# Kernel tuning notes

Measured on AMD Instinct MI355X. Metric: run time of the kernel, lower is better.

Reference implementation:

```python
import jax, jax.numpy as jnp
import numpy as np

IN_FEATURES = 8192
OUT_FEATURES = 8192
BATCH = 64


def setup_inputs() -> dict:
    key = jax.random.key(0)
    k_x, k_mu = jax.random.split(key)
    x = jax.random.normal(k_x, (BATCH, IN_FEATURES), dtype=jnp.float32)
    # torch init: mu = rand(in,1) * out_features; sigma = ones*10; amplitude = ones; bias = zeros
    mu = jax.random.uniform(k_mu, (IN_FEATURES, 1), dtype=jnp.float32) * OUT_FEATURES
    sigma = jnp.ones((IN_FEATURES, 1), dtype=jnp.float32) * 10.0
    amplitude = jnp.ones((IN_FEATURES, 1), dtype=jnp.float32)
    bias = jnp.zeros((OUT_FEATURES,), dtype=jnp.float32)
    return {"x": x, "mu": mu, "sigma": sigma, "amplitude": amplitude, "bias": bias}


def reference(x, mu, sigma, amplitude, bias):
    out_features = bias.shape[0]
    positions = jnp.arange(out_features, dtype=x.dtype)[None, :]  # [1, out]
    diff = positions - mu                                          # [in, out]
    weight = amplitude * jnp.exp(-(diff * diff) / (2.0 * sigma * sigma))  # [in, out]
    out = x @ weight                                               # [B, out]
    return jax.nn.relu(out + bias)
```

## Files before the change

kernel.cpp:

```cpp
#include <hip/hip_runtime.h>

#define IN_F 8192
#define OUT_F 8192
#define BATCH 64
#define PASS 2048
#define TQ 64
#define CH 64

__global__ __launch_bounds__(256) void transpose_x_kern(const float* __restrict__ x,
                                                        float* __restrict__ xT) {
    __shared__ float tile[64][65];
    const int i0 = blockIdx.x * 64;
    const int tid = threadIdx.x;
#pragma unroll
    for (int u = tid; u < 64 * 64; u += 256) {
        const int b = u >> 6;
        const int i = u & 63;
        tile[i][b] = x[b * IN_F + i0 + i];
    }
    __syncthreads();
#pragma unroll
    for (int u = tid; u < 64 * 64; u += 256) {
        const int i = u >> 6;
        const int b = u & 63;
        xT[(i0 + i) * 64 + b] = tile[i][b];
    }
}

__global__ __launch_bounds__(256) void gauss_fc_kern(
    const float* __restrict__ x, const float* __restrict__ xT,
    const float* __restrict__ mu, const float* __restrict__ sigma,
    const float* __restrict__ amp, const float* __restrict__ bias,
    float* __restrict__ out, const int use_xt) {

    __shared__ float lmu[PASS];
    __shared__ float lk[PASS];
    __shared__ float lamp[PASS];
    __shared__ int   li[PASS];
    __shared__ float xs[CH][16];
    __shared__ int   cnt;

    const int tid = threadIdx.x;
    const int c = tid & 63;
    const int g = tid >> 6;
    const int tile0 = blockIdx.x * TQ;
    const int row0 = blockIdx.y * 16;
    const float colf = (float)(tile0 + c);
    const float lo = (float)tile0;
    const float hi = (float)(tile0 + TQ - 1);

    float acc0 = 0.f, acc1 = 0.f, acc2 = 0.f, acc3 = 0.f;

    for (int base = 0; base < IN_F; base += PASS) {
        if (tid == 0) cnt = 0;
        __syncthreads();

        for (int i = base + tid; i < base + PASS; i += 256) {
            const float m = mu[i];
            const float s = sigma[i];
            const float R = 8.0f * fabsf(s) + 1.0f;
            if (m >= lo - R && m <= hi + R) {
                const int p = atomicAdd(&cnt, 1);
                lmu[p] = m;
                lk[p] = -0.5f / (s * s);
                lamp[p] = amp[i];
                li[p] = i;
            }
        }
        __syncthreads();
        const int n = cnt;

        for (int cb = 0; cb < n; cb += CH) {
            const int cn = min(CH, n - cb);
            for (int u = tid; u < (cn << 4); u += 256) {
                const int ci = u >> 4;
                const int r = u & 15;
                const int i = li[cb + ci];
                xs[ci][r] = use_xt ? xT[i * 64 + row0 + r]
                                   : x[(row0 + r) * IN_F + i];
            }
            __syncthreads();

            const int g4 = g << 2;
#pragma unroll 4
            for (int j = 0; j < cn; ++j) {
                const float m = lmu[cb + j];
                const float k = lk[cb + j];
                const float a = lamp[cb + j];
                const float d = colf - m;
                const float w = a * __expf(k * d * d);
                acc0 += w * xs[j][g4 + 0];
                acc1 += w * xs[j][g4 + 1];
                acc2 += w * xs[j][g4 + 2];
                acc3 += w * xs[j][g4 + 3];
            }
            __syncthreads();
        }
    }

    const float bb = bias[tile0 + c];
    float* o = out + (size_t)(row0 + (g << 2)) * OUT_F + tile0 + c;
    float v0 = acc0 + bb;
    float v1 = acc1 + bb;
    float v2 = acc2 + bb;
    float v3 = acc3 + bb;
    o[0 * (size_t)OUT_F] = v0 > 0.f ? v0 : 0.f;
    o[1 * (size_t)OUT_F] = v1 > 0.f ? v1 : 0.f;
    o[2 * (size_t)OUT_F] = v2 > 0.f ? v2 : 0.f;
    o[3 * (size_t)OUT_F] = v3 > 0.f ? v3 : 0.f;
}

extern "C" void kernel_launch(void* const* d_in, const int* in_sizes, int n_in,
                              void* d_out, int out_size, void* d_ws, size_t ws_size,
                              hipStream_t stream) {
    const float* x     = (const float*)d_in[0];
    const float* mu    = (const float*)d_in[1];
    const float* sigma = (const float*)d_in[2];
    const float* amp   = (const float*)d_in[3];
    const float* bias  = (const float*)d_in[4];
    float* out = (float*)d_out;

    const size_t xt_bytes = (size_t)IN_F * BATCH * sizeof(float);
    const int use_xt = (ws_size >= xt_bytes) ? 1 : 0;
    float* xT = (float*)d_ws;

    if (use_xt) {
        transpose_x_kern<<<IN_F / 64, 256, 0, stream>>>(x, xT);
    }
    dim3 grid(OUT_F / TQ, 4);
    gauss_fc_kern<<<grid, 256, 0, stream>>>(x, xT, mu, sigma, amp, bias, out, use_xt);
}
```

Baseline: 97.49 us.

## Halve output tile width to double block count and vectorize mu/sigma scan

Shrinks each block's output column tile from 64 to 32, so twice as many blocks run and each thread keeps 2 batch-row accumulators instead of 4. Loads mu and sigma as float4 in the candidate-filter scan and adds a launch-bounds occupancy hint. The goal is more parallelism across CUs and a cheaper filter scan. The cost is that each Gaussian's exp is now computed per 2 rows instead of 4, so exp work per output grows, and the mu/sigma scan is repeated by twice as many blocks.

```diff
diff --git a/kernel.cpp b/kernel.cpp
--- a/kernel.cpp
+++ b/kernel.cpp
@@ -4,7 +4,8 @@
 #define OUT_F 8192
 #define BATCH 64
 #define PASS 2048
-#define TQ 64
+#define TQ 32
+#define ROWS 16
 #define CH 64
 
 __global__ __launch_bounds__(256) void transpose_x_kern(const float* __restrict__ x,
@@ -27,9 +28,9 @@
     }
 }
 
-__global__ __launch_bounds__(256) void gauss_fc_kern(
+__global__ __launch_bounds__(256, 4) void gauss_fc_kern(
     const float* __restrict__ x, const float* __restrict__ xT,
-    const float* __restrict__ mu, const float* __restrict__ sigma,
+    const float4* __restrict__ mu4, const float4* __restrict__ sg4,
     const float* __restrict__ amp, const float* __restrict__ bias,
     float* __restrict__ out, const int use_xt) {
 
@@ -37,34 +38,43 @@
     __shared__ float lk[PASS];
     __shared__ float lamp[PASS];
     __shared__ int   li[PASS];
-    __shared__ float xs[CH][16];
+    __shared__ float xs[CH][ROWS];
     __shared__ int   cnt;
 
     const int tid = threadIdx.x;
-    const int c = tid & 63;
-    const int g = tid >> 6;
+    const int c = tid & 31;
+    const int g = tid >> 5;
     const int tile0 = blockIdx.x * TQ;
-    const int row0 = blockIdx.y * 16;
+    const int row0 = blockIdx.y * ROWS;
     const float colf = (float)(tile0 + c);
     const float lo = (float)tile0;
     const float hi = (float)(tile0 + TQ - 1);
 
-    float acc0 = 0.f, acc1 = 0.f, acc2 = 0.f, acc3 = 0.f;
+    float acc0 = 0.f, acc1 = 0.f;
 
     for (int base = 0; base < IN_F; base += PASS) {
         if (tid == 0) cnt = 0;
         __syncthreads();
 
-        for (int i = base + tid; i < base + PASS; i += 256) {
-            const float m = mu[i];
-            const float s = sigma[i];
-            const float R = 8.0f * fabsf(s) + 1.0f;
-            if (m >= lo - R && m <= hi + R) {
-                const int p = atomicAdd(&cnt, 1);
-                lmu[p] = m;
-                lk[p] = -0.5f / (s * s);
-                lamp[p] = amp[i];
-                li[p] = i;
+        const int q_end = (base + PASS) >> 2;
+        for (int q = (base >> 2) + tid; q < q_end; q += 256) {
+            const float4 m4 = mu4[q];
+            const float4 s4 = sg4[q];
+            const float ms[4] = {m4.x, m4.y, m4.z, m4.w};
+            const float ss[4] = {s4.x, s4.y, s4.z, s4.w};
+#pragma unroll
+            for (int e = 0; e < 4; ++e) {
+                const float m = ms[e];
+                const float s = ss[e];
+                const float R = 8.0f * fabsf(s) + 1.0f;
+                if (m >= lo - R && m <= hi + R) {
+                    const int i = (q << 2) + e;
+                    const int p = atomicAdd(&cnt, 1);
+                    lmu[p] = m;
+                    lk[p] = -0.5f / (s * s);
+                    lamp[p] = amp[i];
+                    li[p] = i;
+                }
             }
         }
         __syncthreads();
@@ -77,37 +87,28 @@
                 const int r = u & 15;
                 const int i = li[cb + ci];
                 xs[ci][r] = use_xt ? xT[i * 64 + row0 + r]
-                                   : x[(row0 + r) * IN_F + i];
+                                   : x[(size_t)(row0 + r) * IN_F + i];
             }
             __syncthreads();
 
-            const int g4 = g << 2;
+            const int g2 = g << 1;
 #pragma unroll 4
             for (int j = 0; j < cn; ++j) {
-                const float m = lmu[cb + j];
-                const float k = lk[cb + j];
-                const float a = lamp[cb + j];
-                const float d = colf - m;
-                const float w = a * __expf(k * d * d);
-                acc0 += w * xs[j][g4 + 0];
-                acc1 += w * xs[j][g4 + 1];
-                acc2 += w * xs[j][g4 + 2];
-                acc3 += w * xs[j][g4 + 3];
+                const float d = colf - lmu[cb + j];
+                const float w = lamp[cb + j] * __expf(lk[cb + j] * d * d);
+                acc0 += w * xs[j][g2 + 0];
+                acc1 += w * xs[j][g2 + 1];
             }
             __syncthreads();
         }
     }
 
     const float bb = bias[tile0 + c];
-    float* o = out + (size_t)(row0 + (g << 2)) * OUT_F + tile0 + c;
-    float v0 = acc0 + bb;
-    float v1 = acc1 + bb;
-    float v2 = acc2 + bb;
-    float v3 = acc3 + bb;
-    o[0 * (size_t)OUT_F] = v0 > 0.f ? v0 : 0.f;
-    o[1 * (size_t)OUT_F] = v1 > 0.f ? v1 : 0.f;
-    o[2 * (size_t)OUT_F] = v2 > 0.f ? v2 : 0.f;
-    o[3 * (size_t)OUT_F] = v3 > 0.f ? v3 : 0.f;
+    const int r0 = row0 + (g << 1);
+    const float v0 = acc0 + bb;
+    const float v1 = acc1 + bb;
+    out[(size_t)r0 * OUT_F + tile0 + c]       = v0 > 0.f ? v0 : 0.f;
+    out[(size_t)(r0 + 1) * OUT_F + tile0 + c] = v1 > 0.f ? v1 : 0.f;
 }
 
 extern "C" void kernel_launch(void* const* d_in, const int* in_sizes, int n_in,
@@ -127,6 +128,8 @@
     if (use_xt) {
         transpose_x_kern<<<IN_F / 64, 256, 0, stream>>>(x, xT);
     }
-    dim3 grid(OUT_F / TQ, 4);
-    gauss_fc_kern<<<grid, 256, 0, stream>>>(x, xT, mu, sigma, amp, bias, out, use_xt);
+    dim3 grid(OUT_F / TQ, BATCH / ROWS);
+    gauss_fc_kern<<<grid, 256, 0, stream>>>(x, xT,
+                                            (const float4*)mu, (const float4*)sigma,
+                                            amp, bias, out, use_xt);
 }
```

New measurement: 95.90 us. Within noise of the previous version (-1.6%).
